# Kernel tuning notes

Measured on AMD Instinct MI355X. Metric: run time of the kernel, lower is better.

Reference implementation:

```python
import jax, jax.numpy as jnp
import numpy as np

B, N, D, H, LH, AH = 4, 2048, 512, 4, 64, 64
NUM_BUCKETS = 128
EPS = 1e-6
LENGTHS = np.array([2048, 1536, 1024, 1792])  # jagged per-sequence lengths, sum = 6400


def _ln(x, eps=EPS):
    # F.layer_norm without affine params (biased variance)
    m = jnp.mean(x, axis=-1, keepdims=True)
    v = jnp.var(x, axis=-1, keepdims=True)
    return (x - m) * jax.lax.rsqrt(v + eps)


def _rel_bias(all_timestamps, ts_w):
    # bucketed time-delta relative attention bias -> [B, N, N]
    delta = (all_timestamps[:, :, None] - all_timestamps[:, None, :]).astype(jnp.float32)
    bucket = jnp.clip(jnp.floor(jnp.log1p(jnp.abs(delta))).astype(jnp.int32), 0, NUM_BUCKETS)
    return ts_w[bucket]


def setup_inputs() -> dict:
    key = jax.random.key(0)
    ks = jax.random.split(key, 6)
    offsets = np.concatenate([[0], np.cumsum(LENGTHS)]).astype(np.int32)
    T = int(offsets[-1])
    token_batch = np.repeat(np.arange(B), LENGTHS).astype(np.int32)
    token_pos = np.concatenate([np.arange(l) for l in LENGTHS]).astype(np.int32)
    x = jax.random.normal(ks[0], (T, D), jnp.float32)
    uvqk = jax.random.normal(ks[1], (D, 2 * LH * H + 2 * AH * H), jnp.float32) * 0.02
    o_w = jax.random.normal(ks[2], (D, LH * H), jnp.float32) * 0.02  # torch Linear weight [out, in]
    o_b = jnp.zeros((D,), jnp.float32)
    ts_w = jax.random.normal(ks[3], (NUM_BUCKETS + 1,), jnp.float32) * 0.02
    all_timestamps = jnp.sort(jax.random.randint(ks[4], (B, N), 0, 1000000, jnp.int32), axis=-1)
    invalid_attn_mask = jnp.tril(jnp.ones((N, N), jnp.float32))  # causal validity mask in {0,1}
    return {
        'x': x, 'uvqk': uvqk, 'o_w': o_w, 'o_b': o_b, 'ts_w': ts_w,
        'all_timestamps': all_timestamps, 'invalid_attn_mask': invalid_attn_mask,
        'x_offsets': jnp.asarray(offsets), 'token_batch': jnp.asarray(token_batch),
        'token_pos': jnp.asarray(token_pos),
    }


def reference(x, uvqk, o_w, o_b, ts_w, all_timestamps, invalid_attn_mask,
              x_offsets, token_batch, token_pos):
    # input layernorm + fused uvqk projection with SiLU
    h = jax.nn.silu(_ln(x) @ uvqk)  # [T, 2*H*LH + 2*H*AH]
    u, v, q, k = jnp.split(h, [LH * H, 2 * LH * H, 2 * LH * H + AH * H], axis=1)

    def pad(vals):  # jagged [T, d] -> padded dense [B, N, d]
        return jnp.zeros((B, N, vals.shape[-1]), vals.dtype).at[token_batch, token_pos].set(vals)

    pq = pad(q).reshape(B, N, H, AH)
    pk = pad(k).reshape(B, N, H, AH)
    pv = pad(v).reshape(B, N, H, LH)

    scores = jnp.einsum('bnhd,bmhd->bhnm', pq, pk)
    scores = scores + _rel_bias(all_timestamps, ts_w)[:, None]  # broadcast over heads
    scores = jax.nn.silu(scores) / N
    scores = scores * invalid_attn_mask[None, None]
    attn = jnp.einsum('bhnm,bmhd->bnhd', scores, pv).reshape(B, N, H * LH)
    attn_j = attn[token_batch, token_pos]  # dense -> jagged [T, H*LH]

    o_in = u * _ln(attn_j)
    return o_in @ o_w.T + o_b + x
```

## Files before the change

### kernel.cpp

```cpp
#include <hip/hip_runtime.h>
#include <math.h>


typedef __attribute__((ext_vector_type(8))) short bf16x8;
typedef __attribute__((ext_vector_type(4))) float f32x4;

__device__ __forceinline__ float silu_over_2048(float v) {
    return v * __builtin_amdgcn_rcpf(2048.0f + 2048.0f * __expf(-v));
}

__device__ __forceinline__ float silu_f(float v) {
    return v * __builtin_amdgcn_rcpf(1.0f + __expf(-v));
}

__device__ __forceinline__ unsigned short f2bf(float f) {
    unsigned int u = __float_as_uint(f);
    u += 0x7fffu + ((u >> 16) & 1u);
    return (unsigned short)(u >> 16);
}

__device__ __forceinline__ unsigned int f2bf2(float lo, float hi) {
#if __has_builtin(__builtin_amdgcn_cvt_pk_bf16_f32)
    typedef __attribute__((ext_vector_type(2))) short bf16x2;
    bf16x2 p = __builtin_amdgcn_cvt_pk_bf16_f32(lo, hi);
    return *(unsigned int*)&p;
#else
    return (unsigned int)f2bf(lo) | ((unsigned int)f2bf(hi) << 16);
#endif
}

__device__ __forceinline__ void gload_lds16(const unsigned short* g, unsigned short* l) {
    __builtin_amdgcn_global_load_lds(
        (const __attribute__((address_space(1))) void*)(g),
        (__attribute__((address_space(3))) void*)(l),
        16, 0, 0);
}

__global__ __launch_bounds__(256) void k1_ln_prep(const float* __restrict__ x,
                                                  unsigned short* __restrict__ xnb,
                                                  const float* __restrict__ uvqk,
                                                  unsigned short* __restrict__ uvqkT,
                                                  const float* __restrict__ ow,
                                                  unsigned short* __restrict__ owb) {
    const int tid = threadIdx.x;
    const int bx = blockIdx.x;
    if (bx < 1600) {
        const int row = bx * 4 + (tid >> 6);
        const int lane = tid & 63;
        const float* xr = x + row * 512 + lane * 8;
        const float4 v0 = *(const float4*)xr;
        const float4 v1 = *(const float4*)(xr + 4);
        float s = v0.x + v0.y + v0.z + v0.w + v1.x + v1.y + v1.z + v1.w;
        float ss = v0.x * v0.x + v0.y * v0.y + v0.z * v0.z + v0.w * v0.w +
                   v1.x * v1.x + v1.y * v1.y + v1.z * v1.z + v1.w * v1.w;
#pragma unroll
        for (int off = 32; off > 0; off >>= 1) {
            s += __shfl_down(s, off);
            ss += __shfl_down(ss, off);
        }
        s = __shfl(s, 0);
        ss = __shfl(ss, 0);
        const float mean = s * (1.0f / 512.0f);
        const float var = ss * (1.0f / 512.0f) - mean * mean;
        const float rstd = rsqrtf(var + 1e-6f);
        unsigned int pk[4];
        pk[0] = f2bf2((v0.x - mean) * rstd, (v0.y - mean) * rstd);
        pk[1] = f2bf2((v0.z - mean) * rstd, (v0.w - mean) * rstd);
        pk[2] = f2bf2((v1.x - mean) * rstd, (v1.y - mean) * rstd);
        pk[3] = f2bf2((v1.z - mean) * rstd, (v1.w - mean) * rstd);
        *(uint4*)(xnb + row * 512 + lane * 8) = *(const uint4*)pk;
    } else if (bx < 1728) {
        __shared__ float L[64][68];
        const int t = bx - 1600;
        const int n0 = (t & 15) * 64;
        const int k0 = (t >> 4) * 64;
#pragma unroll
        for (int i = 0; i < 4; ++i) {
            const int r = (tid >> 4) + i * 16;
            const int c = (tid & 15) * 4;
            *(float4*)&L[r][c] = *(const float4*)(uvqk + (k0 + r) * 1024 + n0 + c);
        }
        __syncthreads();
        const int n = tid >> 2;
        const int kb = (tid & 3) * 16;
#pragma unroll
        for (int pass = 0; pass < 2; ++pass) {
            unsigned short pk[8];
#pragma unroll
            for (int j = 0; j < 8; ++j) pk[j] = f2bf(L[kb + pass * 8 + j][n]);
            *(uint4*)(uvqkT + (n0 + n) * 512 + k0 + kb + pass * 8) = *(const uint4*)pk;
        }
    } else {
        const int base = ((bx - 1728) * 256 + tid) * 8;
        float4 a = *(const float4*)(ow + base);
        float4 b = *(const float4*)(ow + base + 4);
        unsigned short pk[8] = {f2bf(a.x), f2bf(a.y), f2bf(a.z), f2bf(a.w),
                                f2bf(b.x), f2bf(b.y), f2bf(b.z), f2bf(b.w)};
        *(uint4*)(owb + base) = *(const uint4*)pk;
    }
}

__global__ __launch_bounds__(256, 4) void k2_gemm1(const unsigned short* __restrict__ A,
                                                   const unsigned short* __restrict__ Bt,
                                                   float* __restrict__ u_out,
                                                   unsigned short* __restrict__ hb,
                                                   unsigned short* __restrict__ vtb) {
    __shared__ __align__(16) unsigned short smem[8192];
    unsigned short* As = smem;
    unsigned short* Bs = smem + 4096;
    const int tid = threadIdx.x;
    const int lane = tid & 63;
    const int w = tid >> 6;
    const int l15 = lane & 15;
    const int quad = lane >> 4;
    const int bm = blockIdx.y * 64;
    const int bn = blockIdx.x * 64;

    const int srow = lane >> 3;
    const int scol = ((lane & 7) ^ srow) * 8;
    const unsigned short* gA = A + (size_t)(bm + w * 8 + srow) * 512 + scol;
    const unsigned short* gB = Bt + (size_t)(bn + w * 8 + srow) * 512 + scol;

    const int xA = (l15 & 7) << 3;
    f32x4 acc[4] = {};
    for (int kc = 0; kc < 512; kc += 64) {
        __syncthreads();
#pragma unroll
        for (int i = 0; i < 2; ++i) {
            gload_lds16(gA + (size_t)(i * 32) * 512 + kc, As + (w + i * 4) * 512);
            gload_lds16(gB + (size_t)(i * 32) * 512 + kc, Bs + (w + i * 4) * 512);
        }
        __syncthreads();
        const bf16x8 a0 = *(const bf16x8*)&As[(w * 16 + l15) * 64 + ((quad * 8) ^ xA)];
        const bf16x8 a1 = *(const bf16x8*)&As[(w * 16 + l15) * 64 + ((32 + quad * 8) ^ xA)];
#pragma unroll
        for (int nt = 0; nt < 4; ++nt) {
            bf16x8 b0 = *(const bf16x8*)&Bs[(nt * 16 + l15) * 64 + ((quad * 8) ^ xA)];
            bf16x8 b1 = *(const bf16x8*)&Bs[(nt * 16 + l15) * 64 + ((32 + quad * 8) ^ xA)];
            acc[nt] = __builtin_amdgcn_mfma_f32_16x16x32_bf16(a0, b0, acc[nt], 0, 0, 0);
            acc[nt] = __builtin_amdgcn_mfma_f32_16x16x32_bf16(a1, b1, acc[nt], 0, 0, 0);
        }
    }
    const int m = bm + w * 16 + quad * 4;
    if (bn < 256) {
#pragma unroll
        for (int nt = 0; nt < 4; ++nt)
#pragma unroll
            for (int reg = 0; reg < 4; ++reg)
                u_out[(m + reg) * 256 + bn + nt * 16 + l15] = silu_f(acc[nt][reg]);
    } else if (bn < 512) {
        unsigned short(*T)[72] = (unsigned short(*)[72])smem;
        __syncthreads();
#pragma unroll
        for (int nt = 0; nt < 4; ++nt) {
            unsigned int p01 = f2bf2(silu_f(acc[nt][0]), silu_f(acc[nt][1]));
            unsigned int p23 = f2bf2(silu_f(acc[nt][2]), silu_f(acc[nt][3]));
            unsigned int pk2[2] = {p01, p23};
            *(uint2*)&T[nt * 16 + l15][w * 16 + quad * 4] = *(const uint2*)pk2;
        }
        __syncthreads();
        const int sr = tid >> 3, sc = (tid & 7) * 8;
#pragma unroll
        for (int i = 0; i < 2; ++i) {
            const int r = sr + i * 32;
            *(uint4*)(vtb + (size_t)(bn - 256 + r) * 6400 + bm + sc) = *(const uint4*)&T[r][sc];
        }
    } else {
#pragma unroll
        for (int nt = 0; nt < 4; ++nt) {
            unsigned int p01 = f2bf2(silu_f(acc[nt][0]), silu_f(acc[nt][1]));
            unsigned int p23 = f2bf2(silu_f(acc[nt][2]), silu_f(acc[nt][3]));
            unsigned short* hp = hb + (size_t)m * 768 + (bn - 256) + nt * 16 + l15;
            hp[0] = (unsigned short)p01;
            hp[768] = (unsigned short)(p01 >> 16);
            hp[1536] = (unsigned short)p23;
            hp[2304] = (unsigned short)(p23 >> 16);
        }
    }
}

__global__ __launch_bounds__(256, 5) void k3_attn(const unsigned short* __restrict__ hb,
                                                  const unsigned short* __restrict__ vtb,
                                                  const int* __restrict__ ts,
                                                  const float* __restrict__ tsw,
                                                  const int* __restrict__ offs,
                                                  float* __restrict__ part) {
    const int qt = 31 - (blockIdx.x & 31);
    const int c = blockIdx.x >> 5;
    const int b = blockIdx.y;
    const int hd = blockIdx.z;
    const int off = offs[b];
    const int len = offs[b + 1] - off;
    const int nqt = len >> 6;
    if (qt >= nqt || c * 4 > qt) return;
    const int q0 = qt * 64;
    const int kt_lo = c * 4;
    const int kt_hi = min(qt, c * 4 + 3);

    __shared__ __align__(16) unsigned short QPs[64][72];
    __shared__ __align__(16) unsigned short Ks[64][72];
    __shared__ __align__(16) unsigned short Vt[64][72];
    __shared__ float tqf[64], tkf[64];
    __shared__ float tw[132];

    const int tid = threadIdx.x;
    const int lane = tid & 63;
    const int w = tid >> 6;
    const int l15 = lane & 15;
    const int quad = lane >> 4;
    const int sr = tid >> 3;
    const int sc = (tid & 7) * 8;

    if (tid < 129) tw[tid] = tsw[tid];
    if (tid < 64) tqf[tid] = (float)ts[b * 2048 + q0 + tid];
#pragma unroll
    for (int i = 0; i < 2; ++i)
        *(uint4*)&QPs[sr + i * 32][sc] =
            *(const uint4*)(hb + (off + q0 + sr + i * 32) * 768 + 256 + hd * 64 + sc);
    __syncthreads();

    const bf16x8 aQ0 = *(const bf16x8*)&QPs[w * 16 + l15][quad * 8];
    const bf16x8 aQ1 = *(const bf16x8*)&QPs[w * 16 + l15][32 + quad * 8];
    const f32x4 tq4 = *(const f32x4*)&tqf[w * 16 + quad * 4];
    const int nbase = q0 + w * 16 + quad * 4;

    f32x4 oacc[4] = {};

    for (int kt = kt_lo; kt <= kt_hi; ++kt) {
        const int m0 = kt * 64;
        __syncthreads();
#pragma unroll
        for (int i = 0; i < 2; ++i) {
            const int r = sr + i * 32;
            *(uint4*)&Ks[r][sc] =
                *(const uint4*)(hb + (off + m0 + r) * 768 + 512 + hd * 64 + sc);
            *(uint4*)&Vt[r][sc] =
                *(const uint4*)(vtb + (size_t)(hd * 64 + r) * 6400 + off + m0 + sc);
        }
        if (tid < 64) tkf[tid] = (float)ts[b * 2048 + m0 + tid];
        __syncthreads();

        f32x4 s[4] = {};
#pragma unroll
        for (int nt = 0; nt < 4; ++nt) {
            bf16x8 b0 = *(const bf16x8*)&Ks[nt * 16 + l15][quad * 8];
            bf16x8 b1 = *(const bf16x8*)&Ks[nt * 16 + l15][32 + quad * 8];
            s[nt] = __builtin_amdgcn_mfma_f32_16x16x32_bf16(aQ0, b0, s[nt], 0, 0, 0);
            s[nt] = __builtin_amdgcn_mfma_f32_16x16x32_bf16(aQ1, b1, s[nt], 0, 0, 0);
        }

        const bool diag = (kt == qt);
#pragma unroll
        for (int nt = 0; nt < 4; ++nt) {
            const int m = m0 + nt * 16 + l15;
            const float tk = tkf[nt * 16 + l15];
            float p[4];
#pragma unroll
            for (int reg = 0; reg < 4; ++reg) {
                const float delta = fabsf(tq4[reg] - tk);
                const int bucket = (int)(__log2f(1.0f + delta) * 0.6931471805599453f);
                float val = s[nt][reg] + tw[bucket];
                float pv = silu_over_2048(val);
                if (diag) pv = (m <= nbase + reg) ? pv : 0.0f;
                p[reg] = pv;
            }
            const unsigned int p01 = f2bf2(p[0], p[1]);
            const unsigned int p23 = f2bf2(p[2], p[3]);
            QPs[w * 16 + quad * 4 + 0][nt * 16 + l15] = (unsigned short)p01;
            QPs[w * 16 + quad * 4 + 1][nt * 16 + l15] = (unsigned short)(p01 >> 16);
            QPs[w * 16 + quad * 4 + 2][nt * 16 + l15] = (unsigned short)p23;
            QPs[w * 16 + quad * 4 + 3][nt * 16 + l15] = (unsigned short)(p23 >> 16);
        }

        const bf16x8 aP0 = *(const bf16x8*)&QPs[w * 16 + l15][quad * 8];
        const bf16x8 aP1 = *(const bf16x8*)&QPs[w * 16 + l15][32 + quad * 8];
#pragma unroll
        for (int nt = 0; nt < 4; ++nt) {
            bf16x8 v0 = *(const bf16x8*)&Vt[nt * 16 + l15][quad * 8];
            bf16x8 v1 = *(const bf16x8*)&Vt[nt * 16 + l15][32 + quad * 8];
            oacc[nt] = __builtin_amdgcn_mfma_f32_16x16x32_bf16(aP0, v0, oacc[nt], 0, 0, 0);
            oacc[nt] = __builtin_amdgcn_mfma_f32_16x16x32_bf16(aP1, v1, oacc[nt], 0, 0, 0);
        }
    }

    float* pc = part + (size_t)c * (6400 * 256);
#pragma unroll
    for (int nt = 0; nt < 4; ++nt)
#pragma unroll
        for (int reg = 0; reg < 4; ++reg)
            pc[(off + q0 + w * 16 + quad * 4 + reg) * 256 + hd * 64 + nt * 16 + l15] =
                oacc[nt][reg];
}

__global__ __launch_bounds__(256) void k4a_ln(const float* __restrict__ part,
                                              const float* __restrict__ u_in,
                                              const int* __restrict__ token_pos,
                                              unsigned short* __restrict__ o_in) {
    const int row = blockIdx.x;
    const int tid = threadIdx.x;
    const int qt = token_pos[row] >> 6;
    const int nch = (qt + 4) >> 2;
    float a = 0.0f;
    for (int c = 0; c < nch; ++c) a += part[(size_t)c * (6400 * 256) + row * 256 + tid];
    float s = a, ss = a * a;
#pragma unroll
    for (int off = 32; off > 0; off >>= 1) {
        s += __shfl_down(s, off);
        ss += __shfl_down(ss, off);
    }
    __shared__ float red[8];
    if ((tid & 63) == 0) { red[tid >> 6] = s; red[4 + (tid >> 6)] = ss; }
    __syncthreads();
    s = red[0] + red[1] + red[2] + red[3];
    ss = red[4] + red[5] + red[6] + red[7];
    const float mean = s * (1.0f / 256.0f);
    const float var = ss * (1.0f / 256.0f) - mean * mean;
    const float rstd = rsqrtf(var + 1e-6f);
    const float u = u_in[row * 256 + tid];
    o_in[row * 256 + tid] = f2bf(u * (a - mean) * rstd);
}

__global__ __launch_bounds__(256, 4) void k4b_gemm2(const unsigned short* __restrict__ A,
                                                    const unsigned short* __restrict__ owb,
                                                    const float* __restrict__ ob,
                                                    const float* __restrict__ x,
                                                    float* __restrict__ out) {
    __shared__ __align__(16) unsigned short smem[8192];
    unsigned short* As = smem;
    unsigned short* Bs = smem + 4096;
    const int tid = threadIdx.x;
    const int lane = tid & 63;
    const int w = tid >> 6;
    const int l15 = lane & 15;
    const int quad = lane >> 4;
    const int bm = blockIdx.y * 64;
    const int bn = blockIdx.x * 64;

    const int srow = lane >> 3;
    const int scol = ((lane & 7) ^ srow) * 8;
    const unsigned short* gA = A + (size_t)(bm + w * 8 + srow) * 256 + scol;
    const unsigned short* gB = owb + (size_t)(bn + w * 8 + srow) * 256 + scol;

    const int xA = (l15 & 7) << 3;
    f32x4 acc[4] = {};
    for (int kc = 0; kc < 256; kc += 64) {
        __syncthreads();
#pragma unroll
        for (int i = 0; i < 2; ++i) {
            gload_lds16(gA + (size_t)(i * 32) * 256 + kc, As + (w + i * 4) * 512);
            gload_lds16(gB + (size_t)(i * 32) * 256 + kc, Bs + (w + i * 4) * 512);
        }
        __syncthreads();
        const bf16x8 a0 = *(const bf16x8*)&As[(w * 16 + l15) * 64 + ((quad * 8) ^ xA)];
        const bf16x8 a1 = *(const bf16x8*)&As[(w * 16 + l15) * 64 + ((32 + quad * 8) ^ xA)];
#pragma unroll
        for (int nt = 0; nt < 4; ++nt) {
            bf16x8 b0 = *(const bf16x8*)&Bs[(nt * 16 + l15) * 64 + ((quad * 8) ^ xA)];
            bf16x8 b1 = *(const bf16x8*)&Bs[(nt * 16 + l15) * 64 + ((32 + quad * 8) ^ xA)];
            acc[nt] = __builtin_amdgcn_mfma_f32_16x16x32_bf16(a0, b0, acc[nt], 0, 0, 0);
            acc[nt] = __builtin_amdgcn_mfma_f32_16x16x32_bf16(a1, b1, acc[nt], 0, 0, 0);
        }
    }
    const int m = bm + w * 16 + quad * 4;
#pragma unroll
    for (int nt = 0; nt < 4; ++nt) {
        const int d = bn + nt * 16 + l15;
        const float bias = ob[d];
#pragma unroll
        for (int reg = 0; reg < 4; ++reg)
            out[(m + reg) * 512 + d] = acc[nt][reg] + bias + x[(m + reg) * 512 + d];
    }
}

extern "C" void kernel_launch(void* const* d_in, const int* in_sizes, int n_in,
                              void* d_out, int out_size, void* d_ws, size_t ws_size,
                              hipStream_t stream) {
    const float* x = (const float*)d_in[0];
    const float* uvqk = (const float*)d_in[1];
    const float* ow = (const float*)d_in[2];
    const float* ob = (const float*)d_in[3];
    const float* tsw = (const float*)d_in[4];
    const int* ts = (const int*)d_in[5];
    const int* offs = (const int*)d_in[7];
    const int* token_pos = (const int*)d_in[9];
    float* out = (float*)d_out;

    float* ws = (float*)d_ws;
    float* u = ws;
    float* part = u + 6400 * 256;
    unsigned short* xnb = (unsigned short*)(part + 8 * 6400 * 256);
    unsigned short* hb = xnb + 6400 * 512;
    unsigned short* o_in = hb + 6400 * 768;
    unsigned short* uvqkT = o_in + 6400 * 256;
    unsigned short* owb = uvqkT + 1024 * 512;
    unsigned short* vtb = owb + 512 * 256;

    k1_ln_prep<<<1792, 256, 0, stream>>>(x, xnb, uvqk, uvqkT, ow, owb);
    k2_gemm1<<<dim3(16, 100), 256, 0, stream>>>(xnb, uvqkT, u, hb, vtb);
    k3_attn<<<dim3(256, 4, 4), 256, 0, stream>>>(hb, vtb, ts, tsw, offs, part);
    k4a_ln<<<6400, 256, 0, stream>>>(part, u, token_pos, o_in);
    k4b_gemm2<<<dim3(8, 100), 256, 0, stream>>>(o_in, owb, ob, x, out);
}
```

Before: 157.2 us.

## Remap attention blocks per XCD by batch, vectorize LN, use nontemporal stores

The attention grid is flattened to 1D, and each block index is remapped so that blocks of the same batch land on a fixed subset of the 8 XCDs, in proportion to sequence length, with the longest query tiles scheduled first. This improves L2 locality of K/V reuse and load balance. The LN kernel now handles four rows per block, one wavefront per row, using float4 nontemporal loads and shuffles instead of a shared-memory reduction. Stores of u and the partial accumulators become nontemporal to reduce cache pollution. The gains rely on the hardware's round-robin assignment of blocks to XCDs.

```diff
diff --git a/kernel.cpp b/kernel.cpp
--- a/kernel.cpp
+++ b/kernel.cpp
@@ -147,7 +147,8 @@
         for (int nt = 0; nt < 4; ++nt)
 #pragma unroll
             for (int reg = 0; reg < 4; ++reg)
-                u_out[(m + reg) * 256 + bn + nt * 16 + l15] = silu_f(acc[nt][reg]);
+                __builtin_nontemporal_store(silu_f(acc[nt][reg]),
+                                            &u_out[(m + reg) * 256 + bn + nt * 16 + l15]);
     } else if (bn < 512) {
         unsigned short(*T)[72] = (unsigned short(*)[72])smem;
         __syncthreads();
@@ -185,14 +186,21 @@
                                                   const float* __restrict__ tsw,
                                                   const int* __restrict__ offs,
                                                   float* __restrict__ part) {
-    const int qt = 31 - (blockIdx.x & 31);
-    const int c = blockIdx.x >> 5;
-    const int b = blockIdx.y;
-    const int hd = blockIdx.z;
+    const int xcd = blockIdx.x & 7;
+    const int slot = blockIdx.x >> 3;
+    const int b = (xcd < 3) ? 0 : (xcd < 5) ? 1 : (xcd == 5) ? 2 : 3;
+    const int xst = (b == 0) ? 0 : (b == 1) ? 3 : (b == 2) ? 5 : 6;
+    const int kx = (b == 0) ? 3 : (b == 2) ? 1 : 2;
+    const int r = slot * kx + (xcd - xst);
     const int off = offs[b];
     const int len = offs[b + 1] - off;
     const int nqt = len >> 6;
-    if (qt >= nqt || c * 4 > qt) return;
+    const int qt_lpt = r >> 5;
+    if (qt_lpt >= nqt) return;
+    const int qt = nqt - 1 - qt_lpt;
+    const int c = (r >> 2) & 7;
+    const int hd = r & 3;
+    if (c * 4 > qt) return;
     const int q0 = qt * 64;
     const int kt_lo = c * 4;
     const int kt_hi = min(qt, c * 4 + 3);
@@ -231,11 +239,11 @@
         __syncthreads();
 #pragma unroll
         for (int i = 0; i < 2; ++i) {
-            const int r = sr + i * 32;
-            *(uint4*)&Ks[r][sc] =
-                *(const uint4*)(hb + (off + m0 + r) * 768 + 512 + hd * 64 + sc);
-            *(uint4*)&Vt[r][sc] =
-                *(const uint4*)(vtb + (size_t)(hd * 64 + r) * 6400 + off + m0 + sc);
+            const int r2 = sr + i * 32;
+            *(uint4*)&Ks[r2][sc] =
+                *(const uint4*)(hb + (off + m0 + r2) * 768 + 512 + hd * 64 + sc);
+            *(uint4*)&Vt[r2][sc] =
+                *(const uint4*)(vtb + (size_t)(hd * 64 + r2) * 6400 + off + m0 + sc);
         }
         if (tid < 64) tkf[tid] = (float)ts[b * 2048 + m0 + tid];
         __syncthreads();
@@ -288,36 +296,43 @@
     for (int nt = 0; nt < 4; ++nt)
 #pragma unroll
         for (int reg = 0; reg < 4; ++reg)
-            pc[(off + q0 + w * 16 + quad * 4 + reg) * 256 + hd * 64 + nt * 16 + l15] =
-                oacc[nt][reg];
+            __builtin_nontemporal_store(
+                oacc[nt][reg],
+                &pc[(off + q0 + w * 16 + quad * 4 + reg) * 256 + hd * 64 + nt * 16 + l15]);
 }
 
 __global__ __launch_bounds__(256) void k4a_ln(const float* __restrict__ part,
                                               const float* __restrict__ u_in,
                                               const int* __restrict__ token_pos,
                                               unsigned short* __restrict__ o_in) {
-    const int row = blockIdx.x;
-    const int tid = threadIdx.x;
+    const int row = blockIdx.x * 4 + (threadIdx.x >> 6);
+    const int lane = threadIdx.x & 63;
     const int qt = token_pos[row] >> 6;
     const int nch = (qt + 4) >> 2;
-    float a = 0.0f;
-    for (int c = 0; c < nch; ++c) a += part[(size_t)c * (6400 * 256) + row * 256 + tid];
-    float s = a, ss = a * a;
+    const size_t base = (size_t)row * 256 + lane * 4;
+    f32x4 a = {0.0f, 0.0f, 0.0f, 0.0f};
+    for (int cc = 0; cc < nch; ++cc) {
+        const f32x4 p =
+            __builtin_nontemporal_load((const f32x4*)(part + (size_t)cc * (6400 * 256) + base));
+        a += p;
+    }
+    float s = a[0] + a[1] + a[2] + a[3];
+    float ss = a[0] * a[0] + a[1] * a[1] + a[2] * a[2] + a[3] * a[3];
 #pragma unroll
     for (int off = 32; off > 0; off >>= 1) {
         s += __shfl_down(s, off);
         ss += __shfl_down(ss, off);
     }
-    __shared__ float red[8];
-    if ((tid & 63) == 0) { red[tid >> 6] = s; red[4 + (tid >> 6)] = ss; }
-    __syncthreads();
-    s = red[0] + red[1] + red[2] + red[3];
-    ss = red[4] + red[5] + red[6] + red[7];
+    s = __shfl(s, 0);
+    ss = __shfl(ss, 0);
     const float mean = s * (1.0f / 256.0f);
     const float var = ss * (1.0f / 256.0f) - mean * mean;
     const float rstd = rsqrtf(var + 1e-6f);
-    const float u = u_in[row * 256 + tid];
-    o_in[row * 256 + tid] = f2bf(u * (a - mean) * rstd);
+    const f32x4 uu = __builtin_nontemporal_load((const f32x4*)(u_in + base));
+    unsigned int pk[2];
+    pk[0] = f2bf2(uu[0] * (a[0] - mean) * rstd, uu[1] * (a[1] - mean) * rstd);
+    pk[1] = f2bf2(uu[2] * (a[2] - mean) * rstd, uu[3] * (a[3] - mean) * rstd);
+    *(uint2*)(o_in + base) = *(const uint2*)pk;
 }
 
 __global__ __launch_bounds__(256, 4) void k4b_gemm2(const unsigned short* __restrict__ A,
@@ -397,7 +412,7 @@
 
     k1_ln_prep<<<1792, 256, 0, stream>>>(x, xnb, uvqk, uvqkT, ow, owb);
     k2_gemm1<<<dim3(16, 100), 256, 0, stream>>>(xnb, uvqkT, u, hb, vtb);
-    k3_attn<<<dim3(256, 4, 4), 256, 0, stream>>>(hb, vtb, ts, tsw, offs, part);
-    k4a_ln<<<6400, 256, 0, stream>>>(part, u, token_pos, o_in);
+    k3_attn<<<4096, 256, 0, stream>>>(hb, vtb, ts, tsw, offs, part);
+    k4a_ln<<<1600, 256, 0, stream>>>(part, u, token_pos, o_in);
     k4b_gemm2<<<dim3(8, 100), 256, 0, stream>>>(o_in, owb, ob, x, out);
 }
```

Result: faster. 149.5 us (-4.8%).
